# Kernel optimization log

Measured on AMD Instinct MI355X. Metric: run time of the kernel, lower is better.

The kernel has to match this reference:

```python
import jax, jax.numpy as jnp
import numpy as np

H = 768
K_NORMAL = 3  # {B, I, O}
K_TS = 7      # {B-POS,B-NEG,B-NEU,I-POS,I-NEG,I-NEU,O}
EPSILON = 0.5


def build_w_trans():
    # ote_vocab: B=0, I=1, O=2 ; ts_vocab: B-POS=0,B-NEG=1,B-NEU=2,I-POS=3,I-NEG=4,I-NEU=5,O=6
    w = np.zeros((K_NORMAL, K_TS), dtype=np.float32)
    w[0, 0:3] = 1.0 / 3.0  # B -> B-POS/B-NEG/B-NEU
    w[1, 3:6] = 1.0 / 3.0  # I -> I-POS/I-NEG/I-NEU
    w[2, 6] = 1.0          # O -> O
    return jnp.asarray(w)


def crf_log_likelihood(emissions, tags, mask, trans, start, end):
    """Linear-chain CRF log-likelihood, summed over the batch.
    emissions: [B,T,K] float, tags: [B,T] int, mask: [B,T] int (first step valid).
    """
    B, T, K = emissions.shape
    maskf = mask.astype(emissions.dtype)
    # gold score
    emit = jnp.take_along_axis(emissions, tags[..., None], axis=2)[..., 0]  # [B,T]
    emit_score = jnp.sum(emit * maskf, axis=1)
    tr = trans[tags[:, :-1], tags[:, 1:]]  # [B,T-1]
    trans_score = jnp.sum(tr * maskf[:, 1:], axis=1)
    last_idx = jnp.sum(mask, axis=1).astype(jnp.int32) - 1  # [B]
    last_tag = jnp.take_along_axis(tags, last_idx[:, None], axis=1)[:, 0]
    score = emit_score + trans_score + start[tags[:, 0]] + end[last_tag]
    # partition function via forward algorithm (scan over time)
    alpha0 = start[None, :] + emissions[:, 0]  # [B,K]
    emits_t = jnp.moveaxis(emissions[:, 1:], 1, 0)        # [T-1,B,K]
    mask_t = jnp.moveaxis(mask[:, 1:].astype(bool), 1, 0)  # [T-1,B]

    def step(alpha, inp):
        e, m = inp
        nxt = jax.nn.logsumexp(alpha[:, :, None] + trans[None, :, :] + e[:, None, :], axis=1)
        return jnp.where(m[:, None], nxt, alpha), None

    alphaT, _ = jax.lax.scan(step, alpha0, (emits_t, mask_t))
    logZ = jax.nn.logsumexp(alphaT + end[None, :], axis=1)  # [B]
    return jnp.sum(score - logZ)


def setup_inputs() -> dict:
    key = jax.random.key(0)
    ks = jax.random.split(key, 12)
    B, T = 64, 512
    x = jax.random.normal(ks[0], (B, T, H), dtype=jnp.float32)
    attention_mask = jnp.ones((B, T), dtype=jnp.int32)
    labels = jax.random.randint(ks[1], (B, T), 0, K_TS, dtype=jnp.int32)
    labels_normal = jax.random.randint(ks[2], (B, T), 0, K_NORMAL, dtype=jnp.int32)
    s = 1.0 / np.sqrt(H)
    params = {
        'w_normal': jax.random.uniform(ks[3], (H, K_NORMAL), minval=-s, maxval=s),
        'b_normal': jax.random.uniform(ks[4], (K_NORMAL,), minval=-s, maxval=s),
        'w_upper': jax.random.uniform(ks[5], (H, K_TS), minval=-s, maxval=s),
        'b_upper': jax.random.uniform(ks[6], (K_TS,), minval=-s, maxval=s),
        'trans_n': jax.random.uniform(ks[7], (K_NORMAL, K_NORMAL), minval=-0.1, maxval=0.1),
        'start_n': jax.random.uniform(ks[8], (K_NORMAL,), minval=-0.1, maxval=0.1),
        'end_n': jax.random.uniform(ks[8], (K_NORMAL,), minval=-0.1, maxval=0.1) * 0.5,
        'trans_s': jax.random.uniform(ks[9], (K_TS, K_TS), minval=-0.1, maxval=0.1),
        'start_s': jax.random.uniform(ks[10], (K_TS,), minval=-0.1, maxval=0.1),
        'end_s': jax.random.uniform(ks[11], (K_TS,), minval=-0.1, maxval=0.1),
        'w_trans': build_w_trans(),
    }
    return {'x': x, 'attention_mask': attention_mask, 'labels': labels,
            'labels_normal': labels_normal, **params}


def reference(x, attention_mask, labels, labels_normal,
              w_normal, b_normal, w_upper, b_upper,
              trans_n, start_n, end_n, trans_s, start_s, end_s, w_trans):
    z_t = x @ w_normal + b_normal  # [B,T,Kn]
    loss = -crf_log_likelihood(z_t, labels_normal, attention_mask, trans_n, start_n, end_n)
    p = jax.nn.softmax(z_t, axis=2)
    alpha = EPSILON * jnp.sum(p * p, axis=2)  # [B,T]
    z_s = x @ w_upper + b_upper               # [B,T,Ks]
    z_s_prime = z_t @ w_trans                 # [B,T,Ks]
    z_s_tilde = z_s_prime * alpha[..., None] + z_s * (1.0 - alpha[..., None])
    loss = loss - crf_log_likelihood(z_s_tilde, labels, attention_mask, trans_s, start_s, end_s)
    return (loss, z_s_tilde)
```

## Files before the change

kernel.cpp:

```cpp
#include <hip/hip_runtime.h>
#include <math.h>

#define T_SEQ 512
#define B_SZ  64
#define HDIM  768
#define NROWS (B_SZ * T_SEQ)
#define NEGI  (-1e30f)

__global__ __launch_bounds__(256) void k1_fused_linear(
    const float* __restrict__ x,
    const float* __restrict__ w_normal, const float* __restrict__ b_normal,
    const float* __restrict__ w_upper,  const float* __restrict__ b_upper,
    const float* __restrict__ w_trans,
    float* __restrict__ zst_out,
    float* __restrict__ zt_out)
{
    const int lane = threadIdx.x & 63;
    const int wid  = blockIdx.x * (blockDim.x >> 6) + (threadIdx.x >> 6);
    const int nw   = gridDim.x * (blockDim.x >> 6);

    float wN[3][4][3];
    float wU[3][4][7];
#pragma unroll
    for (int i = 0; i < 3; ++i) {
#pragma unroll
        for (int j = 0; j < 4; ++j) {
            const int h = i * 256 + lane * 4 + j;
#pragma unroll
            for (int k = 0; k < 3; ++k) wN[i][j][k] = w_normal[h * 3 + k];
#pragma unroll
            for (int k = 0; k < 7; ++k) wU[i][j][k] = w_upper[h * 7 + k];
        }
    }
    float bn[3], bu[7], wt[3][7];
#pragma unroll
    for (int k = 0; k < 3; ++k) bn[k] = b_normal[k];
#pragma unroll
    for (int k = 0; k < 7; ++k) bu[k] = b_upper[k];
#pragma unroll
    for (int j = 0; j < 3; ++j)
#pragma unroll
        for (int k = 0; k < 7; ++k) wt[j][k] = w_trans[j * 7 + k];

    for (int row = wid; row < NROWS; row += nw) {
        const float4* xp = reinterpret_cast<const float4*>(x + (size_t)row * HDIM);
        float acc[10];
#pragma unroll
        for (int k = 0; k < 10; ++k) acc[k] = 0.f;
#pragma unroll
        for (int i = 0; i < 3; ++i) {
            const float4 v = xp[i * 64 + lane];
            const float xs0 = v.x, xs1 = v.y, xs2 = v.z, xs3 = v.w;
#pragma unroll
            for (int k = 0; k < 3; ++k) {
                acc[k] += xs0 * wN[i][0][k];
                acc[k] += xs1 * wN[i][1][k];
                acc[k] += xs2 * wN[i][2][k];
                acc[k] += xs3 * wN[i][3][k];
            }
#pragma unroll
            for (int k = 0; k < 7; ++k) {
                acc[3 + k] += xs0 * wU[i][0][k];
                acc[3 + k] += xs1 * wU[i][1][k];
                acc[3 + k] += xs2 * wU[i][2][k];
                acc[3 + k] += xs3 * wU[i][3][k];
            }
        }
#pragma unroll
        for (int off = 32; off >= 1; off >>= 1) {
#pragma unroll
            for (int k = 0; k < 10; ++k)
                acc[k] += __shfl_xor(acc[k], off, 64);
        }
        const float zt0 = acc[0] + bn[0];
        const float zt1 = acc[1] + bn[1];
        const float zt2 = acc[2] + bn[2];
        const float mx = fmaxf(zt0, fmaxf(zt1, zt2));
        const float e0 = __expf(zt0 - mx);
        const float e1 = __expf(zt1 - mx);
        const float e2 = __expf(zt2 - mx);
        const float inv = 1.0f / (e0 + e1 + e2);
        const float p0 = e0 * inv, p1 = e1 * inv, p2 = e2 * inv;
        const float alpha = 0.5f * (p0 * p0 + p1 * p1 + p2 * p2);
        const float oma = 1.0f - alpha;
        float zst[7];
#pragma unroll
        for (int k = 0; k < 7; ++k) {
            const float zs  = acc[3 + k] + bu[k];
            const float zsp = zt0 * wt[0][k] + zt1 * wt[1][k] + zt2 * wt[2][k];
            zst[k] = zsp * alpha + zs * oma;
        }
        float vsel = zst[0];
#pragma unroll
        for (int k = 1; k < 7; ++k) vsel = (lane == k) ? zst[k] : vsel;
        if (lane < 7) zst_out[(size_t)row * 7 + lane] = vsel;
        const float vt = (lane == 8) ? zt1 : ((lane == 9) ? zt2 : zt0);
        if (lane >= 7 && lane < 10) zt_out[(size_t)row * 3 + (lane - 7)] = vt;
    }
}

template <int K>
__device__ __forceinline__ void crf_chunk(
    const float* __restrict__ e_base,
    const int*   __restrict__ mask,
    const float* __restrict__ trans,
    int c, int irow,
    float* __restrict__ outrow)
{
    float tr[K][K];
#pragma unroll
    for (int i = 0; i < K; ++i)
#pragma unroll
        for (int j = 0; j < K; ++j) tr[i][j] = trans[i * K + j];

    float a[K];
#pragma unroll
    for (int j = 0; j < K; ++j) a[j] = (j == irow) ? 0.f : NEGI;

    const int t0 = 1 + c * 8;
    int t1 = t0 + 8;
    if (t1 > T_SEQ) t1 = T_SEQ;
    for (int t = t0; t < t1; ++t) {
        if (mask[t]) {
            float e[K];
#pragma unroll
            for (int j = 0; j < K; ++j) e[j] = e_base[t * K + j];
            float na[K];
#pragma unroll
            for (int j = 0; j < K; ++j) {
                float m = a[0] + tr[0][j];
#pragma unroll
                for (int i = 1; i < K; ++i) m = fmaxf(m, a[i] + tr[i][j]);
                float s = 0.f;
#pragma unroll
                for (int i = 0; i < K; ++i) s += __expf(a[i] + tr[i][j] - m);
                na[j] = e[j] + m + __logf(s);
            }
#pragma unroll
            for (int j = 0; j < K; ++j) a[j] = na[j];
        }
    }
#pragma unroll
    for (int j = 0; j < K; ++j) outrow[j] = a[j];
}

__global__ __launch_bounds__(256) void k2_chunks(
    const float* __restrict__ zst, const float* __restrict__ zt,
    const int* __restrict__ mask,
    const float* __restrict__ trans_s, const float* __restrict__ trans_n,
    float* __restrict__ M7, float* __restrict__ M3)
{
    const int tid = blockIdx.x * 256 + threadIdx.x;
    const int N7 = B_SZ * 64 * 7;
    if (tid < N7) {
        const int i = tid % 7;
        const int c = (tid / 7) & 63;
        const int b = tid / (7 * 64);
        crf_chunk<7>(zst + (size_t)b * T_SEQ * 7, mask + b * T_SEQ, trans_s,
                     c, i, M7 + ((size_t)(b * 64 + c) * 7 + i) * 7);
    } else if (tid < N7 + B_SZ * 64 * 3) {
        const int r = tid - N7;
        const int i = r % 3;
        const int c = (r / 3) & 63;
        const int b = r / (3 * 64);
        crf_chunk<3>(zt + (size_t)b * T_SEQ * 3, mask + b * T_SEQ, trans_n,
                     c, i, M3 + ((size_t)(b * 64 + c) * 3 + i) * 3);
    }
}

template <int K>
__device__ void combine_and_score(
    const float* __restrict__ M,
    const float* __restrict__ z,
    const int*   __restrict__ mask,
    const int*   __restrict__ labels,
    const float* __restrict__ trans, const float* __restrict__ startv,
    const float* __restrict__ endv,
    float* __restrict__ out_partial,
    float* bufA, float* bufB, float* red, float* redm)
{
    const int tid = threadIdx.x;
    const int KK = K * K;
    for (int idx = tid; idx < 64 * KK; idx += 256) bufA[idx] = M[idx];
    __syncthreads();

    float* src = bufA;
    float* dst = bufB;
    int n = 64;
    while (n > 1) {
        const int half = n >> 1;
        const int tasks = half * KK;
        for (int task = tid; task < tasks; task += 256) {
            const int p = task / KK;
            const int ij = task % KK;
            const int i = ij / K, j = ij % K;
            const float* A  = src + (size_t)(2 * p) * KK;
            const float* Bm = src + (size_t)(2 * p + 1) * KK;
            float m = A[i * K + 0] + Bm[0 * K + j];
#pragma unroll
            for (int k = 1; k < K; ++k) m = fmaxf(m, A[i * K + k] + Bm[k * K + j]);
            float s = 0.f;
#pragma unroll
            for (int k = 0; k < K; ++k) s += __expf(A[i * K + k] + Bm[k * K + j] - m);
            dst[task] = m + __logf(s);
        }
        __syncthreads();
        float* tmp = src; src = dst; dst = tmp;
        n = half;
    }

    float local_s = 0.f, local_m = 0.f;
    for (int t = tid; t < T_SEQ; t += 256) {
        const float mf = (float)mask[t];
        const int tg = labels[t];
        local_s += mf * z[t * K + tg];
        local_m += mf;
        if (t >= 1) {
            const int tp = labels[t - 1];
            local_s += mf * trans[tp * K + tg];
        }
    }
    red[tid] = local_s;
    redm[tid] = local_m;
    __syncthreads();
    for (int s = 128; s >= 1; s >>= 1) {
        if (tid < s) { red[tid] += red[tid + s]; redm[tid] += redm[tid + s]; }
        __syncthreads();
    }
    if (tid == 0) {
        float score = red[0];
        const int nvalid = (int)(redm[0] + 0.5f);
        const int last = nvalid - 1;
        score += startv[labels[0]] + endv[labels[last]];

        float alpha0[K];
#pragma unroll
        for (int i = 0; i < K; ++i) alpha0[i] = startv[i] + z[i];
        float v[K];
#pragma unroll
        for (int j = 0; j < K; ++j) {
            float m = alpha0[0] + src[0 * K + j];
#pragma unroll
            for (int i = 1; i < K; ++i) m = fmaxf(m, alpha0[i] + src[i * K + j]);
            float s = 0.f;
#pragma unroll
            for (int i = 0; i < K; ++i) s += __expf(alpha0[i] + src[i * K + j] - m);
            v[j] = m + __logf(s) + endv[j];
        }
        float mm = v[0];
#pragma unroll
        for (int j = 1; j < K; ++j) mm = fmaxf(mm, v[j]);
        float ss = 0.f;
#pragma unroll
        for (int j = 0; j < K; ++j) ss += __expf(v[j] - mm);
        const float logZ = mm + __logf(ss);
        out_partial[0] = score - logZ;
    }
}

__global__ __launch_bounds__(256) void k3_combine(
    const float* __restrict__ M7, const float* __restrict__ M3,
    const float* __restrict__ zst, const float* __restrict__ zt,
    const int* __restrict__ mask, const int* __restrict__ labels,
    const int* __restrict__ labels_n,
    const float* __restrict__ trans_s, const float* __restrict__ start_s,
    const float* __restrict__ end_s,
    const float* __restrict__ trans_n, const float* __restrict__ start_n,
    const float* __restrict__ end_n,
    float* __restrict__ partials)
{
    __shared__ float bufA[64 * 49];
    __shared__ float bufB[32 * 49];
    __shared__ float red[256];
    __shared__ float redm[256];
    const int b = blockIdx.x & 63;
    if (blockIdx.x < 64) {
        combine_and_score<3>(M3 + (size_t)b * 64 * 9, zt + (size_t)b * T_SEQ * 3,
                             mask + b * T_SEQ, labels_n + b * T_SEQ,
                             trans_n, start_n, end_n, partials + blockIdx.x,
                             bufA, bufB, red, redm);
    } else {
        combine_and_score<7>(M7 + (size_t)b * 64 * 49, zst + (size_t)b * T_SEQ * 7,
                             mask + b * T_SEQ, labels + b * T_SEQ,
                             trans_s, start_s, end_s, partials + blockIdx.x,
                             bufA, bufB, red, redm);
    }
}

__global__ __launch_bounds__(128) void k4_reduce(const float* __restrict__ partials,
                                                 float* __restrict__ out0)
{
    __shared__ float red[128];
    const int tid = threadIdx.x;
    red[tid] = partials[tid];
    __syncthreads();
    for (int s = 64; s >= 1; s >>= 1) {
        if (tid < s) red[tid] += red[tid + s];
        __syncthreads();
    }
    if (tid == 0) out0[0] = -red[0];
}

extern "C" void kernel_launch(void* const* d_in, const int* in_sizes, int n_in,
                              void* d_out, int out_size, void* d_ws, size_t ws_size,
                              hipStream_t stream)
{
    const float* x        = (const float*)d_in[0];
    const int*   mask     = (const int*)d_in[1];
    const int*   labels   = (const int*)d_in[2];
    const int*   labels_n = (const int*)d_in[3];
    const float* w_normal = (const float*)d_in[4];
    const float* b_normal = (const float*)d_in[5];
    const float* w_upper  = (const float*)d_in[6];
    const float* b_upper  = (const float*)d_in[7];
    const float* trans_n  = (const float*)d_in[8];
    const float* start_n  = (const float*)d_in[9];
    const float* end_n    = (const float*)d_in[10];
    const float* trans_s  = (const float*)d_in[11];
    const float* start_s  = (const float*)d_in[12];
    const float* end_s    = (const float*)d_in[13];
    const float* w_trans  = (const float*)d_in[14];

    float* out      = (float*)d_out;
    float* loss_out = out;
    float* zst      = out + 1;

    float* ws       = (float*)d_ws;
    float* zt       = ws;
    float* M7       = ws + 98304;
    float* M3       = ws + 98304 + 200704;
    float* partials = ws + 98304 + 200704 + 36864;

    k1_fused_linear<<<2048, 256, 0, stream>>>(x, w_normal, b_normal, w_upper,
                                              b_upper, w_trans, zst, zt);
    k2_chunks<<<160, 256, 0, stream>>>(zst, zt, mask, trans_s, trans_n, M7, M3);
    k3_combine<<<128, 256, 0, stream>>>(M7, M3, zst, zt, mask, labels, labels_n,
                                        trans_s, start_s, end_s,
                                        trans_n, start_n, end_n, partials);
    k4_reduce<<<1, 128, 0, stream>>>(partials, loss_out);
}
```

Baseline: 65.23 us.

## Fuse CRF chunk and combine kernels, prefetch rows in linear kernel, atomic loss

The linear kernel now stages the weights through shared memory, runs a fixed grid of 512 blocks, and software-prefetches the next x row into registers while it computes the current one. The separate chunk-scan kernel, combine kernel and final-reduction kernel are merged into one CRF kernel per sequence. Each thread computes its chunk transfer matrix directly into shared memory, using exp(trans) multiplications instead of a per-step logsumexp over pairs. The loss is accumulated with atomicAdd after a memset, which removes two launches and the workspace round trips. The cost is fewer threads working on the CRF chunk stage (only 128 blocks) and a nondeterministic float summation order.

```diff
diff --git a/kernel.cpp b/kernel.cpp
--- a/kernel.cpp
+++ b/kernel.cpp
@@ -7,7 +7,11 @@
 #define NROWS (B_SZ * T_SEQ)
 #define NEGI  (-1e30f)
 
-__global__ __launch_bounds__(256) void k1_fused_linear(
+#define K1_BLOCKS 512
+#define K1_WAVES  (K1_BLOCKS * 4)
+#define ROWS_PER_WAVE (NROWS / K1_WAVES)
+
+__global__ __launch_bounds__(256, 2) void k1_fused_linear(
     const float* __restrict__ x,
     const float* __restrict__ w_normal, const float* __restrict__ b_normal,
     const float* __restrict__ w_upper,  const float* __restrict__ b_upper,
@@ -15,9 +19,14 @@
     float* __restrict__ zst_out,
     float* __restrict__ zt_out)
 {
-    const int lane = threadIdx.x & 63;
-    const int wid  = blockIdx.x * (blockDim.x >> 6) + (threadIdx.x >> 6);
-    const int nw   = gridDim.x * (blockDim.x >> 6);
+    __shared__ float sW[7680];
+    const int tid = threadIdx.x;
+    for (int i = tid; i < 2304; i += 256) sW[i] = w_normal[i];
+    for (int i = tid; i < 5376; i += 256) sW[2304 + i] = w_upper[i];
+    __syncthreads();
+
+    const int lane = tid & 63;
+    const int wid  = blockIdx.x * 4 + (tid >> 6);
 
     float wN[3][4][3];
     float wU[3][4][7];
@@ -27,9 +36,9 @@
         for (int j = 0; j < 4; ++j) {
             const int h = i * 256 + lane * 4 + j;
 #pragma unroll
-            for (int k = 0; k < 3; ++k) wN[i][j][k] = w_normal[h * 3 + k];
-#pragma unroll
-            for (int k = 0; k < 7; ++k) wU[i][j][k] = w_upper[h * 7 + k];
+            for (int k = 0; k < 3; ++k) wN[i][j][k] = sW[h * 3 + k];
+#pragma unroll
+            for (int k = 0; k < 7; ++k) wU[i][j][k] = sW[2304 + h * 7 + k];
         }
     }
     float bn[3], bu[7], wt[3][7];
@@ -42,15 +51,30 @@
 #pragma unroll
         for (int k = 0; k < 7; ++k) wt[j][k] = w_trans[j * 7 + k];
 
-    for (int row = wid; row < NROWS; row += nw) {
+    int row = wid;
+    float4 cur[3];
+    {
         const float4* xp = reinterpret_cast<const float4*>(x + (size_t)row * HDIM);
+        cur[0] = xp[lane]; cur[1] = xp[64 + lane]; cur[2] = xp[128 + lane];
+    }
+
+#pragma unroll 1
+    for (int it = 0; it < ROWS_PER_WAVE; ++it) {
+        const int nrow = row + K1_WAVES;
+        float4 nxt[3];
+        if (it + 1 < ROWS_PER_WAVE) {
+            const float4* np = reinterpret_cast<const float4*>(x + (size_t)nrow * HDIM);
+            nxt[0] = np[lane]; nxt[1] = np[64 + lane]; nxt[2] = np[128 + lane];
+        } else {
+            nxt[0] = cur[0]; nxt[1] = cur[1]; nxt[2] = cur[2];
+        }
+
         float acc[10];
 #pragma unroll
         for (int k = 0; k < 10; ++k) acc[k] = 0.f;
 #pragma unroll
         for (int i = 0; i < 3; ++i) {
-            const float4 v = xp[i * 64 + lane];
-            const float xs0 = v.x, xs1 = v.y, xs2 = v.z, xs3 = v.w;
+            const float xs0 = cur[i].x, xs1 = cur[i].y, xs2 = cur[i].z, xs3 = cur[i].w;
 #pragma unroll
             for (int k = 0; k < 3; ++k) {
                 acc[k] += xs0 * wN[i][0][k];
@@ -96,92 +120,62 @@
         if (lane < 7) zst_out[(size_t)row * 7 + lane] = vsel;
         const float vt = (lane == 8) ? zt1 : ((lane == 9) ? zt2 : zt0);
         if (lane >= 7 && lane < 10) zt_out[(size_t)row * 3 + (lane - 7)] = vt;
+
+        cur[0] = nxt[0]; cur[1] = nxt[1]; cur[2] = nxt[2];
+        row = nrow;
     }
 }
 
 template <int K>
-__device__ __forceinline__ void crf_chunk(
-    const float* __restrict__ e_base,
-    const int*   __restrict__ mask,
-    const float* __restrict__ trans,
-    int c, int irow,
-    float* __restrict__ outrow)
-{
-    float tr[K][K];
-#pragma unroll
-    for (int i = 0; i < K; ++i)
-#pragma unroll
-        for (int j = 0; j < K; ++j) tr[i][j] = trans[i * K + j];
-
-    float a[K];
-#pragma unroll
-    for (int j = 0; j < K; ++j) a[j] = (j == irow) ? 0.f : NEGI;
-
-    const int t0 = 1 + c * 8;
-    int t1 = t0 + 8;
-    if (t1 > T_SEQ) t1 = T_SEQ;
-    for (int t = t0; t < t1; ++t) {
-        if (mask[t]) {
-            float e[K];
-#pragma unroll
-            for (int j = 0; j < K; ++j) e[j] = e_base[t * K + j];
-            float na[K];
-#pragma unroll
-            for (int j = 0; j < K; ++j) {
-                float m = a[0] + tr[0][j];
-#pragma unroll
-                for (int i = 1; i < K; ++i) m = fmaxf(m, a[i] + tr[i][j]);
-                float s = 0.f;
-#pragma unroll
-                for (int i = 0; i < K; ++i) s += __expf(a[i] + tr[i][j] - m);
-                na[j] = e[j] + m + __logf(s);
-            }
-#pragma unroll
-            for (int j = 0; j < K; ++j) a[j] = na[j];
-        }
-    }
-#pragma unroll
-    for (int j = 0; j < K; ++j) outrow[j] = a[j];
-}
-
-__global__ __launch_bounds__(256) void k2_chunks(
-    const float* __restrict__ zst, const float* __restrict__ zt,
-    const int* __restrict__ mask,
-    const float* __restrict__ trans_s, const float* __restrict__ trans_n,
-    float* __restrict__ M7, float* __restrict__ M3)
-{
-    const int tid = blockIdx.x * 256 + threadIdx.x;
-    const int N7 = B_SZ * 64 * 7;
-    if (tid < N7) {
-        const int i = tid % 7;
-        const int c = (tid / 7) & 63;
-        const int b = tid / (7 * 64);
-        crf_chunk<7>(zst + (size_t)b * T_SEQ * 7, mask + b * T_SEQ, trans_s,
-                     c, i, M7 + ((size_t)(b * 64 + c) * 7 + i) * 7);
-    } else if (tid < N7 + B_SZ * 64 * 3) {
-        const int r = tid - N7;
-        const int i = r % 3;
-        const int c = (r / 3) & 63;
-        const int b = r / (3 * 64);
-        crf_chunk<3>(zt + (size_t)b * T_SEQ * 3, mask + b * T_SEQ, trans_n,
-                     c, i, M3 + ((size_t)(b * 64 + c) * 3 + i) * 3);
-    }
-}
-
-template <int K>
-__device__ void combine_and_score(
-    const float* __restrict__ M,
+__device__ void crf_block(
     const float* __restrict__ z,
     const int*   __restrict__ mask,
     const int*   __restrict__ labels,
     const float* __restrict__ trans, const float* __restrict__ startv,
     const float* __restrict__ endv,
-    float* __restrict__ out_partial,
+    float* __restrict__ loss,
     float* bufA, float* bufB, float* red, float* redm)
 {
     const int tid = threadIdx.x;
     const int KK = K * K;
-    for (int idx = tid; idx < 64 * KK; idx += 256) bufA[idx] = M[idx];
+
+    for (int task = tid; task < 64 * K; task += 256) {
+        const int c = task / K;
+        const int irow = task % K;
+        float E[K][K];
+#pragma unroll
+        for (int i = 0; i < K; ++i)
+#pragma unroll
+            for (int j = 0; j < K; ++j) E[i][j] = __expf(trans[i * K + j]);
+        float a[K];
+#pragma unroll
+        for (int j = 0; j < K; ++j) a[j] = (j == irow) ? 0.f : NEGI;
+        const int t0 = 1 + c * 8;
+        int t1 = t0 + 8;
+        if (t1 > T_SEQ) t1 = T_SEQ;
+        for (int t = t0; t < t1; ++t) {
+            if (mask[t]) {
+                float m = a[0];
+#pragma unroll
+                for (int i = 1; i < K; ++i) m = fmaxf(m, a[i]);
+                float ea[K];
+#pragma unroll
+                for (int i = 0; i < K; ++i) ea[i] = __expf(a[i] - m);
+                float na[K];
+#pragma unroll
+                for (int j = 0; j < K; ++j) {
+                    float s = 0.f;
+#pragma unroll
+                    for (int i = 0; i < K; ++i) s += ea[i] * E[i][j];
+                    na[j] = z[t * K + j] + m + __logf(s);
+                }
+#pragma unroll
+                for (int j = 0; j < K; ++j) a[j] = na[j];
+            }
+        }
+#pragma unroll
+        for (int j = 0; j < K; ++j) bufA[c * KK + irow * K + j] = a[j];
+    }
     __syncthreads();
 
     float* src = bufA;
@@ -254,12 +248,11 @@
 #pragma unroll
         for (int j = 0; j < K; ++j) ss += __expf(v[j] - mm);
         const float logZ = mm + __logf(ss);
-        out_partial[0] = score - logZ;
+        atomicAdd(loss, logZ - score);
     }
 }
 
-__global__ __launch_bounds__(256) void k3_combine(
-    const float* __restrict__ M7, const float* __restrict__ M3,
+__global__ __launch_bounds__(256) void k2_crf(
     const float* __restrict__ zst, const float* __restrict__ zt,
     const int* __restrict__ mask, const int* __restrict__ labels,
     const int* __restrict__ labels_n,
@@ -267,7 +260,7 @@
     const float* __restrict__ end_s,
     const float* __restrict__ trans_n, const float* __restrict__ start_n,
     const float* __restrict__ end_n,
-    float* __restrict__ partials)
+    float* __restrict__ loss)
 {
     __shared__ float bufA[64 * 49];
     __shared__ float bufB[32 * 49];
@@ -275,30 +268,14 @@
     __shared__ float redm[256];
     const int b = blockIdx.x & 63;
     if (blockIdx.x < 64) {
-        combine_and_score<3>(M3 + (size_t)b * 64 * 9, zt + (size_t)b * T_SEQ * 3,
-                             mask + b * T_SEQ, labels_n + b * T_SEQ,
-                             trans_n, start_n, end_n, partials + blockIdx.x,
-                             bufA, bufB, red, redm);
+        crf_block<3>(zt + (size_t)b * T_SEQ * 3, mask + b * T_SEQ,
+                     labels_n + b * T_SEQ, trans_n, start_n, end_n,
+                     loss, bufA, bufB, red, redm);
     } else {
-        combine_and_score<7>(M7 + (size_t)b * 64 * 49, zst + (size_t)b * T_SEQ * 7,
-                             mask + b * T_SEQ, labels + b * T_SEQ,
-                             trans_s, start_s, end_s, partials + blockIdx.x,
-                             bufA, bufB, red, redm);
-    }
-}
-
-__global__ __launch_bounds__(128) void k4_reduce(const float* __restrict__ partials,
-                                                 float* __restrict__ out0)
-{
-    __shared__ float red[128];
-    const int tid = threadIdx.x;
-    red[tid] = partials[tid];
-    __syncthreads();
-    for (int s = 64; s >= 1; s >>= 1) {
-        if (tid < s) red[tid] += red[tid + s];
-        __syncthreads();
-    }
-    if (tid == 0) out0[0] = -red[0];
+        crf_block<7>(zst + (size_t)b * T_SEQ * 7, mask + b * T_SEQ,
+                     labels + b * T_SEQ, trans_s, start_s, end_s,
+                     loss, bufA, bufB, red, redm);
+    }
 }
 
 extern "C" void kernel_launch(void* const* d_in, const int* in_sizes, int n_in,
@@ -324,18 +301,14 @@
     float* out      = (float*)d_out;
     float* loss_out = out;
     float* zst      = out + 1;
-
-    float* ws       = (float*)d_ws;
-    float* zt       = ws;
-    float* M7       = ws + 98304;
-    float* M3       = ws + 98304 + 200704;
-    float* partials = ws + 98304 + 200704 + 36864;
-
-    k1_fused_linear<<<2048, 256, 0, stream>>>(x, w_normal, b_normal, w_upper,
-                                              b_upper, w_trans, zst, zt);
-    k2_chunks<<<160, 256, 0, stream>>>(zst, zt, mask, trans_s, trans_n, M7, M3);
-    k3_combine<<<128, 256, 0, stream>>>(M7, M3, zst, zt, mask, labels, labels_n,
-                                        trans_s, start_s, end_s,
-                                        trans_n, start_n, end_n, partials);
-    k4_reduce<<<1, 128, 0, stream>>>(partials, loss_out);
+    float* zt       = (float*)d_ws;
+
+    hipMemsetAsync(loss_out, 0, sizeof(float), stream);
+
+    k1_fused_linear<<<K1_BLOCKS, 256, 0, stream>>>(x, w_normal, b_normal,
+                                                   w_upper, b_upper, w_trans,
+                                                   zst, zt);
+    k2_crf<<<128, 256, 0, stream>>>(zst, zt, mask, labels, labels_n,
+                                    trans_s, start_s, end_s,
+                                    trans_n, start_n, end_n, loss_out);
 }
```

After: 64.81 us. No clear change (-0.6%).
